# Optimization experiments

Measured on AMD Instinct MI355X. Metric: run time of the kernel, lower is better.

The kernel has to match this reference:

```python
import jax, jax.numpy as jnp
import numpy as np

N_NODES = 50000
N_EDGES = 800000
IN_CH = 10
HID = 32
HEADS = 4
OUT_CH = 64
EDIM = 1
NEG_SLOPE = 0.2  # PyG GATv2Conv default
LN_EPS = 1e-5


def _glorot(key, shape):
    fan_in, fan_out = shape[0], shape[-1]
    lim = np.sqrt(6.0 / (fan_in + fan_out))
    return jax.random.uniform(key, shape, jnp.float32, -lim, lim)


def setup_inputs() -> dict:
    key = jax.random.key(0)
    ks = jax.random.split(key, 16)
    x = jax.random.normal(ks[0], (N_NODES, IN_CH), jnp.float32)
    edge_index = jax.random.randint(ks[1], (2, N_EDGES), 0, N_NODES, jnp.int64)
    edge_attr = jax.random.normal(ks[2], (N_EDGES, EDIM), jnp.float32)
    return {
        "x": x,
        "edge_attr": edge_attr,
        "W1l": _glorot(ks[3], (IN_CH, HEADS * HID)),
        "W1r": _glorot(ks[4], (IN_CH, HEADS * HID)),
        "W1e": _glorot(ks[5], (EDIM, HEADS * HID)),
        "att1": _glorot(ks[6], (HEADS, HID)),
        "b1": jnp.zeros((HEADS * HID,), jnp.float32),
        "ln1_g": jnp.ones((HEADS * HID,), jnp.float32),
        "ln1_b": jnp.zeros((HEADS * HID,), jnp.float32),
        "W2l": _glorot(ks[7], (HEADS * HID, OUT_CH)),
        "W2r": _glorot(ks[8], (HEADS * HID, OUT_CH)),
        "W2e": _glorot(ks[9], (EDIM, OUT_CH)),
        "att2": _glorot(ks[10], (1, OUT_CH)),
        "b2": jnp.zeros((OUT_CH,), jnp.float32),
        "ln2_g": jnp.ones((OUT_CH,), jnp.float32),
        "ln2_b": jnp.zeros((OUT_CH,), jnp.float32),
        "edge_index": edge_index,
    }


def gatv2_layer(x, src, dst, edge_attr, Wl, Wr, We, att, bias, heads, ch, concat):
    # GATv2: e_ij = att . leaky_relu(Wl x_i + Wr x_j + We e_ij), softmax over j->i
    n = x.shape[0]
    xl = (x @ Wl).reshape(n, heads, ch)          # target projection [N,H,C]
    xr = (x @ Wr).reshape(n, heads, ch)          # source projection [N,H,C]
    ee = (edge_attr @ We).reshape(-1, heads, ch)  # [E,H,C]
    e = jax.nn.leaky_relu(xl[dst] + xr[src] + ee, NEG_SLOPE)  # [E,H,C]
    logit = jnp.einsum('ehc,hc->eh', e, att)     # [E,H]
    m = jax.ops.segment_max(logit, dst, num_segments=n)       # [N,H]
    expv = jnp.exp(logit - m[dst])
    denom = jax.ops.segment_sum(expv, dst, num_segments=n)    # [N,H]
    alpha = expv / denom[dst]                                  # [E,H]
    out = jax.ops.segment_sum(alpha[:, :, None] * xr[src], dst, num_segments=n)  # [N,H,C]
    out = out.reshape(n, heads * ch) if concat else out.mean(axis=1)
    return out + bias


def layer_norm(h, g, b):
    mu = h.mean(axis=-1, keepdims=True)
    var = ((h - mu) ** 2).mean(axis=-1, keepdims=True)
    return (h - mu) * jax.lax.rsqrt(var + LN_EPS) * g + b


def reference(x, edge_attr, W1l, W1r, W1e, att1, b1, ln1_g, ln1_b,
              W2l, W2r, W2e, att2, b2, ln2_g, ln2_b, edge_index):
    src, dst = edge_index[0], edge_index[1]
    h = gatv2_layer(x, src, dst, edge_attr, W1l, W1r, W1e, att1, b1, HEADS, HID, True)
    h = jax.nn.elu(layer_norm(h, ln1_g, ln1_b))
    # dropout is identity in eval mode
    h = gatv2_layer(h, src, dst, edge_attr, W2l, W2r, W2e, att2, b2, 1, OUT_CH, False)
    h = jax.nn.elu(layer_norm(h, ln2_g, ln2_b))
    return h
```

## Files before the change

kernel.cpp:

```cpp
#include <hip/hip_runtime.h>
#include <math.h>

#define NN 50000
#define NE 800000
#define IN_CH 10
#define NEGS 0.2f
#define LNEPS 1e-5f
#define LOG2E 1.4426950408889634f
#define P1_BLOCKS 12500
#define CH_BLOCKS 782
#define NBUK 196

typedef float f2 __attribute__((ext_vector_type(2)));

__device__ __forceinline__ f2 pkfma(f2 a, f2 b, f2 c) {
    return __builtin_elementwise_fma(a, b, c);
}
__device__ __forceinline__ float dppadd1(float v) {
    int r = __builtin_amdgcn_update_dpp(0, __float_as_int(v), 0xB1, 0xF, 0xF, true);
    return v + __int_as_float(r);
}
__device__ __forceinline__ float dppadd2(float v) {
    int r = __builtin_amdgcn_update_dpp(0, __float_as_int(v), 0x4E, 0xF, 0xF, true);
    return v + __int_as_float(r);
}
__device__ __forceinline__ float swzadd4(float v) {
    return v + __int_as_float(__builtin_amdgcn_ds_swizzle(__float_as_int(v), 0x101F));
}
__device__ __forceinline__ float swzadd8(float v) {
    return v + __int_as_float(__builtin_amdgcn_ds_swizzle(__float_as_int(v), 0x201F));
}
__device__ __forceinline__ float red16g(float v) {
    v = dppadd1(v); v = dppadd2(v); v = swzadd4(v); v = swzadd8(v);
    return v;
}
__device__ __forceinline__ float red32g(float v) {
    v = red16g(v);
    v += __int_as_float(__builtin_amdgcn_ds_swizzle(__float_as_int(v), 0x401F));
    return v;
}

__device__ __forceinline__ unsigned pack_bf16(float a, float b) {
    unsigned ua = __float_as_uint(a);
    unsigned ub = __float_as_uint(b);
    ua = (ua + 0x7FFFu + ((ua >> 16) & 1u)) >> 16;
    ub = (ub + 0x7FFFu + ((ub >> 16) & 1u)) & 0xFFFF0000u;
    return ua | ub;
}
__device__ __forceinline__ float bf_lo(unsigned d) { return __uint_as_float(d << 16); }
__device__ __forceinline__ float bf_hi(unsigned d) { return __uint_as_float(d & 0xFFFF0000u); }

__global__ __launch_bounds__(256) void k_proj1_hist(
    const float* __restrict__ x, const float* __restrict__ Wl,
    const float* __restrict__ Wr, float* __restrict__ xl, unsigned* __restrict__ xrb,
    const int* __restrict__ ei, int* __restrict__ bh) {
    __shared__ int h[256];
    int bI = blockIdx.x;
    if (bI < P1_BLOCKS) {
        int lane = threadIdx.x & 63;
        int n = bI * 4 + (threadIdx.x >> 6);
        int c0 = lane * 2;
        float al0 = 0.f, al1 = 0.f, ar0 = 0.f, ar1 = 0.f;
#pragma unroll
        for (int k = 0; k < IN_CH; ++k) {
            float xv = x[n * IN_CH + k];
            al0 = fmaf(xv, Wl[k * 128 + c0], al0);
            al1 = fmaf(xv, Wl[k * 128 + c0 + 1], al1);
            ar0 = fmaf(xv, Wr[k * 128 + c0], ar0);
            ar1 = fmaf(xv, Wr[k * 128 + c0 + 1], ar1);
        }
        *(float2*)&xl[(size_t)n * 128 + c0] = make_float2(al0, al1);
        xrb[(size_t)n * 64 + lane] = pack_bf16(ar0, ar1);
    } else {
        int t = threadIdx.x, b = bI - P1_BLOCKS;
        h[t] = 0;
        __syncthreads();
        int e0 = b * 1024 + t * 4;
        if (e0 < NE) {
            int4 d4 = *(const int4*)(ei + NE + e0);
            atomicAdd(&h[d4.x >> 8], 1);
            atomicAdd(&h[d4.y >> 8], 1);
            atomicAdd(&h[d4.z >> 8], 1);
            atomicAdd(&h[d4.w >> 8], 1);
        }
        __syncthreads();
        bh[b * 256 + t] = h[t];
    }
}

__global__ __launch_bounds__(256) void k_colscan(
    int* __restrict__ bh, int* __restrict__ coltotal) {
    __shared__ int sh[256];
    int t = threadIdx.x, j = blockIdx.x;
    int v[4];
    int mysum = 0;
#pragma unroll
    for (int i = 0; i < 4; ++i) {
        int r = t * 4 + i;
        v[i] = (r < CH_BLOCKS) ? bh[r * 256 + j] : 0;
        mysum += v[i];
    }
    sh[t] = mysum;
    __syncthreads();
    for (int off = 1; off < 256; off <<= 1) {
        int u = (t >= off) ? sh[t - off] : 0;
        __syncthreads();
        sh[t] += u;
        __syncthreads();
    }
    int ex = sh[t] - mysum;
#pragma unroll
    for (int i = 0; i < 4; ++i) {
        int r = t * 4 + i;
        if (r < CH_BLOCKS) { bh[r * 256 + j] = ex; ex += v[i]; }
    }
    if (t == 255) coltotal[j] = sh[255];
}

__global__ __launch_bounds__(256) void k_coarse(
    const int* __restrict__ ei, const float* __restrict__ ea,
    const int* __restrict__ bh, const int* __restrict__ coltotal,
    int2* __restrict__ coarse) {
    __shared__ int h[256];
    __shared__ int lbase[256];
    __shared__ int sh[256];
    int t = threadIdx.x, b = blockIdx.x;
    int ct = coltotal[t];
    sh[t] = ct;
    __syncthreads();
    for (int off = 1; off < 256; off <<= 1) {
        int u = (t >= off) ? sh[t - off] : 0;
        __syncthreads();
        sh[t] += u;
        __syncthreads();
    }
    h[t] = 0;
    lbase[t] = (sh[t] - ct) + bh[b * 256 + t];
    __syncthreads();
    int e0 = b * 1024 + t * 4;
    if (e0 >= NE) return;
    int4 d4 = *(const int4*)(ei + NE + e0);
    int4 s4 = *(const int4*)(ei + e0);
    float4 a4 = *(const float4*)(ea + e0);
    {
        int bk = d4.x >> 8; int r = atomicAdd(&h[bk], 1);
        coarse[lbase[bk] + r] = make_int2(s4.x | ((d4.x & 255) << 16), __float_as_int(a4.x));
    }
    {
        int bk = d4.y >> 8; int r = atomicAdd(&h[bk], 1);
        coarse[lbase[bk] + r] = make_int2(s4.y | ((d4.y & 255) << 16), __float_as_int(a4.y));
    }
    {
        int bk = d4.z >> 8; int r = atomicAdd(&h[bk], 1);
        coarse[lbase[bk] + r] = make_int2(s4.z | ((d4.z & 255) << 16), __float_as_int(a4.z));
    }
    {
        int bk = d4.w >> 8; int r = atomicAdd(&h[bk], 1);
        coarse[lbase[bk] + r] = make_int2(s4.w | ((d4.w & 255) << 16), __float_as_int(a4.w));
    }
}

__global__ __launch_bounds__(256) void k_fine(
    const int2* __restrict__ coarse, const int* __restrict__ coltotal,
    int* __restrict__ rowstart, int2* __restrict__ cpack) {
    __shared__ int cnt[256];
    __shared__ int pfx[256];
    __shared__ int sh[256];
    __shared__ int bbx[257];
    int t = threadIdx.x, b = blockIdx.x;
    int ct = coltotal[t];
    sh[t] = ct;
    __syncthreads();
    for (int off = 1; off < 256; off <<= 1) {
        int u = (t >= off) ? sh[t - off] : 0;
        __syncthreads();
        sh[t] += u;
        __syncthreads();
    }
    bbx[t] = sh[t] - ct;
    if (t == 255) bbx[256] = sh[255];
    cnt[t] = 0;
    __syncthreads();
    int lo = bbx[b], hi = bbx[b + 1];
    int ecnt = hi - lo;
    for (int i = t; i < ecnt; i += 256) {
        int dl = (coarse[lo + i].x >> 16) & 255;
        atomicAdd(&cnt[dl], 1);
    }
    __syncthreads();
    int v = cnt[t];
    sh[t] = v;
    __syncthreads();
    for (int off = 1; off < 256; off <<= 1) {
        int u = (t >= off) ? sh[t - off] : 0;
        __syncthreads();
        sh[t] += u;
        __syncthreads();
    }
    pfx[t] = sh[t] - v;
    int n0 = b * 256;
    if (n0 + t < NN) rowstart[n0 + t] = lo + (sh[t] - v);
    if (b == 0 && t == 0) rowstart[NN] = NE;
    cnt[t] = 0;
    __syncthreads();
    for (int i = t; i < ecnt; i += 256) {
        int2 c = coarse[lo + i];
        int dl = (c.x >> 16) & 255;
        int r = atomicAdd(&cnt[dl], 1);
        cpack[lo + pfx[dl] + r] = make_int2(c.x & 0xFFFF, c.y);
    }
}

__global__ __launch_bounds__(256) void k_proj2(
    const float* __restrict__ h1, const float* __restrict__ Wl,
    const float* __restrict__ Wr, float* __restrict__ xl2, unsigned* __restrict__ xr2b) {
    __shared__ float sh_h[64][36];
    __shared__ float sh_w[32][128];
    int t = threadIdx.x;
    int cg = t & 15, ng = t >> 4;
    int c0 = cg * 8;
    int nb = blockIdx.x * 64;
    float acc[4][8];
#pragma unroll
    for (int j = 0; j < 4; ++j)
#pragma unroll
        for (int i = 0; i < 8; ++i) acc[j][i] = 0.f;

    for (int kc = 0; kc < 128; kc += 32) {
#pragma unroll
        for (int i = 0; i < 2; ++i) {
            int fi = t + i * 256;
            int nl = fi >> 3, kq = fi & 7;
            int n = nb + nl;
            float4 v = make_float4(0.f, 0.f, 0.f, 0.f);
            if (n < NN) v = *(const float4*)&h1[(size_t)n * 128 + kc + kq * 4];
            *(float4*)&sh_h[nl][kq * 4] = v;
        }
#pragma unroll
        for (int i = 0; i < 4; ++i) {
            int fi = t + i * 256;
            int kl = fi >> 5, col = (fi & 31) * 4;
            const float* src = (col < 64) ? &Wl[(size_t)(kc + kl) * 64 + col]
                                          : &Wr[(size_t)(kc + kl) * 64 + col - 64];
            *(float4*)&sh_w[kl][col] = *(const float4*)src;
        }
        __syncthreads();
#pragma unroll
        for (int kl = 0; kl < 32; kl += 4) {
            float4 hv[4];
#pragma unroll
            for (int j = 0; j < 4; ++j) hv[j] = *(const float4*)&sh_h[ng + j * 16][kl];
#pragma unroll
            for (int kk = 0; kk < 4; ++kk) {
                float4 wa = *(const float4*)&sh_w[kl + kk][c0];
                float4 wb = *(const float4*)&sh_w[kl + kk][c0 + 4];
#pragma unroll
                for (int j = 0; j < 4; ++j) {
                    float hs = kk == 0 ? hv[j].x : kk == 1 ? hv[j].y : kk == 2 ? hv[j].z : hv[j].w;
                    acc[j][0] = fmaf(hs, wa.x, acc[j][0]);
                    acc[j][1] = fmaf(hs, wa.y, acc[j][1]);
                    acc[j][2] = fmaf(hs, wa.z, acc[j][2]);
                    acc[j][3] = fmaf(hs, wa.w, acc[j][3]);
                    acc[j][4] = fmaf(hs, wb.x, acc[j][4]);
                    acc[j][5] = fmaf(hs, wb.y, acc[j][5]);
                    acc[j][6] = fmaf(hs, wb.z, acc[j][6]);
                    acc[j][7] = fmaf(hs, wb.w, acc[j][7]);
                }
            }
        }
        __syncthreads();
    }
    if (cg < 8) {
#pragma unroll
        for (int j = 0; j < 4; ++j) {
            int n = nb + ng + j * 16;
            if (n < NN) {
                *(float4*)&xl2[(size_t)n * 64 + c0] =
                    make_float4(acc[j][0], acc[j][1], acc[j][2], acc[j][3]);
                *(float4*)&xl2[(size_t)n * 64 + c0 + 4] =
                    make_float4(acc[j][4], acc[j][5], acc[j][6], acc[j][7]);
            }
        }
    } else {
        int cc = c0 - 64;
#pragma unroll
        for (int j = 0; j < 4; ++j) {
            int n = nb + ng + j * 16;
            if (n < NN) {
                uint4 pk;
                pk.x = pack_bf16(acc[j][0], acc[j][1]);
                pk.y = pack_bf16(acc[j][2], acc[j][3]);
                pk.z = pack_bf16(acc[j][4], acc[j][5]);
                pk.w = pack_bf16(acc[j][6], acc[j][7]);
                *(uint4*)&xr2b[(size_t)n * 32 + (cc >> 1)] = pk;
            }
        }
    }
}


__global__ __launch_bounds__(256) void k_fused1(
    const int* __restrict__ rs, const int2* __restrict__ cpack,
    const float* __restrict__ xl, const unsigned char* __restrict__ xrb,
    const float* __restrict__ We, const float* __restrict__ att,
    const float* __restrict__ bias, const float* __restrict__ g,
    const float* __restrict__ b, float* __restrict__ h1) {
    int lane = threadIdx.x & 63;
    int n = blockIdx.x * 4 + (threadIdx.x >> 6);
    if (n >= NN) return;
    int half = lane >> 5;
    int l = lane & 31;
    int c0 = l * 4;
    unsigned loff = (unsigned)(l * 8);
    float4 xldf = *(const float4*)&xl[(size_t)n * 128 + c0];
    float4 Wef = *(const float4*)&We[c0];
    float4 atv = *(const float4*)&att[c0];
    f2 xl01 = {xldf.x, xldf.y}, xl23 = {xldf.z, xldf.w};
    f2 We01 = {Wef.x, Wef.y}, We23 = {Wef.z, Wef.w};
    f2 at6a = {atv.x * (0.6f * LOG2E), atv.y * (0.6f * LOG2E)};
    f2 at6b = {atv.z * (0.6f * LOG2E), atv.w * (0.6f * LOG2E)};
    f2 at4a = {atv.x * (0.4f * LOG2E), atv.y * (0.4f * LOG2E)};
    f2 at4b = {atv.z * (0.4f * LOG2E), atv.w * (0.4f * LOG2E)};
    int beg = rs[n], end = rs[n + 1];
    f2 a01[2] = {{0.f, 0.f}, {0.f, 0.f}};
    f2 a23[2] = {{0.f, 0.f}, {0.f, 0.f}};
    float den[2] = {0.f, 0.f};
    for (int p0 = beg; p0 < end; p0 += 8) {
        int2 pk[4];
        bool vv[4];
#pragma unroll
        for (int s = 0; s < 4; ++s) {
            int p = p0 + s * 2 + half;
            vv[s] = p < end;
            pk[s] = cpack[vv[s] ? p : end - 1];
        }
        uint2 dw[4];
#pragma unroll
        for (int s = 0; s < 4; ++s)
            dw[s] = *(const uint2*)(xrb + (unsigned)pk[s].x * 256u + loff);
#pragma unroll
        for (int s = 0; s < 4; ++s) {
            float eav = __int_as_float(pk[s].y);
            f2 x01, x23;
            x01.x = bf_lo(dw[s].x); x01.y = bf_hi(dw[s].x);
            x23.x = bf_lo(dw[s].y); x23.y = bf_hi(dw[s].y);
            f2 ev = {eav, eav};
            f2 u01 = pkfma(ev, We01, xl01) + x01;
            f2 u23 = pkfma(ev, We23, xl23) + x23;
            float dot = fmaf(at6a.x, u01.x, at4a.x * fabsf(u01.x));
            dot = fmaf(at6a.y, u01.y, fmaf(at4a.y, fabsf(u01.y), dot));
            dot = fmaf(at6b.x, u23.x, fmaf(at4b.x, fabsf(u23.x), dot));
            dot = fmaf(at6b.y, u23.y, fmaf(at4b.y, fabsf(u23.y), dot));
            dot = dppadd1(dot);
            dot = dppadd2(dot);
            dot = swzadd4(dot);
            float el = vv[s] ? exp2f(dot) : 0.f;
            int w = s & 1;
            den[w] += el;
            f2 el2 = {el, el};
            a01[w] = pkfma(el2, x01, a01[w]);
            a23[w] = pkfma(el2, x23, a23[w]);
        }
    }
    f2 s01 = a01[0] + a01[1];
    f2 s23 = a23[0] + a23[1];
    float den0 = den[0] + den[1];
    s01.x += __shfl_xor(s01.x, 32);
    s01.y += __shfl_xor(s01.y, 32);
    s23.x += __shfl_xor(s23.x, 32);
    s23.y += __shfl_xor(s23.y, 32);
    den0 += __shfl_xor(den0, 32);
    float inv = den0 > 0.f ? 1.f / den0 : 0.f;
    float4 bv = *(const float4*)&bias[c0];
    float a0 = s01.x * inv + bv.x;
    float a1 = s01.y * inv + bv.y;
    float a2 = s23.x * inv + bv.z;
    float a3 = s23.y * inv + bv.w;
    float mu = red32g(a0 + a1 + a2 + a3) * (1.f / 128.f);
    float d0 = a0 - mu, d1 = a1 - mu, d2 = a2 - mu, d3 = a3 - mu;
    float var = red32g(d0 * d0 + d1 * d1 + d2 * d2 + d3 * d3) * (1.f / 128.f);
    float rsq = rsqrtf(var + LNEPS);
    float4 gv = *(const float4*)&g[c0];
    float4 bb = *(const float4*)&b[c0];
    float o0 = d0 * rsq * gv.x + bb.x;
    float o1 = d1 * rsq * gv.y + bb.y;
    float o2 = d2 * rsq * gv.z + bb.z;
    float o3 = d3 * rsq * gv.w + bb.w;
    o0 = o0 > 0.f ? o0 : __expf(o0) - 1.f;
    o1 = o1 > 0.f ? o1 : __expf(o1) - 1.f;
    o2 = o2 > 0.f ? o2 : __expf(o2) - 1.f;
    o3 = o3 > 0.f ? o3 : __expf(o3) - 1.f;
    if (half == 0)
        *(float4*)&h1[(size_t)n * 128 + c0] = make_float4(o0, o1, o2, o3);
}

__global__ __launch_bounds__(256) void k_fused2(
    const int* __restrict__ rs, const int2* __restrict__ cpack,
    const float* __restrict__ xl2, const unsigned char* __restrict__ xr2b,
    const float* __restrict__ We, const float* __restrict__ att,
    const float* __restrict__ bias, const float* __restrict__ g,
    const float* __restrict__ b, float* __restrict__ out) {
    int lane = threadIdx.x & 63;
    int n = blockIdx.x * 4 + (threadIdx.x >> 6);
    if (n >= NN) return;
    int grp = lane >> 4;
    int l = lane & 15;
    int c0 = l * 4;
    unsigned loff = (unsigned)(l * 8);
    float4 xldf = *(const float4*)&xl2[(size_t)n * 64 + c0];
    float4 Wef = *(const float4*)&We[c0];
    float4 atv = *(const float4*)&att[c0];
    f2 xl01 = {xldf.x, xldf.y}, xl23 = {xldf.z, xldf.w};
    f2 We01 = {Wef.x, Wef.y}, We23 = {Wef.z, Wef.w};
    f2 at6a = {atv.x * (0.6f * LOG2E), atv.y * (0.6f * LOG2E)};
    f2 at6b = {atv.z * (0.6f * LOG2E), atv.w * (0.6f * LOG2E)};
    f2 at4a = {atv.x * (0.4f * LOG2E), atv.y * (0.4f * LOG2E)};
    f2 at4b = {atv.z * (0.4f * LOG2E), atv.w * (0.4f * LOG2E)};
    int beg = rs[n], end = rs[n + 1];
    f2 a01[2] = {{0.f, 0.f}, {0.f, 0.f}};
    f2 a23[2] = {{0.f, 0.f}, {0.f, 0.f}};
    float den[2] = {0.f, 0.f};
    for (int p0 = beg; p0 < end; p0 += 16) {
        int2 pk[4];
        bool vv[4];
#pragma unroll
        for (int s = 0; s < 4; ++s) {
            int p = p0 + s * 4 + grp;
            vv[s] = p < end;
            pk[s] = cpack[vv[s] ? p : end - 1];
        }
        uint2 dw[4];
#pragma unroll
        for (int s = 0; s < 4; ++s)
            dw[s] = *(const uint2*)(xr2b + (unsigned)pk[s].x * 128u + loff);
#pragma unroll
        for (int s = 0; s < 4; ++s) {
            float eav = __int_as_float(pk[s].y);
            f2 x01, x23;
            x01.x = bf_lo(dw[s].x); x01.y = bf_hi(dw[s].x);
            x23.x = bf_lo(dw[s].y); x23.y = bf_hi(dw[s].y);
            f2 ev = {eav, eav};
            f2 u01 = pkfma(ev, We01, xl01) + x01;
            f2 u23 = pkfma(ev, We23, xl23) + x23;
            float dot = fmaf(at6a.x, u01.x, at4a.x * fabsf(u01.x));
            dot = fmaf(at6a.y, u01.y, fmaf(at4a.y, fabsf(u01.y), dot));
            dot = fmaf(at6b.x, u23.x, fmaf(at4b.x, fabsf(u23.x), dot));
            dot = fmaf(at6b.y, u23.y, fmaf(at4b.y, fabsf(u23.y), dot));
            dot = dppadd1(dot);
            dot = dppadd2(dot);
            dot = swzadd4(dot);
            dot = swzadd8(dot);
            float el = vv[s] ? exp2f(dot) : 0.f;
            int w = s & 1;
            den[w] += el;
            f2 el2 = {el, el};
            a01[w] = pkfma(el2, x01, a01[w]);
            a23[w] = pkfma(el2, x23, a23[w]);
        }
    }
    f2 s01 = a01[0] + a01[1];
    f2 s23 = a23[0] + a23[1];
    float den0 = den[0] + den[1];
    s01.x += __shfl_xor(s01.x, 16); s01.x += __shfl_xor(s01.x, 32);
    s01.y += __shfl_xor(s01.y, 16); s01.y += __shfl_xor(s01.y, 32);
    s23.x += __shfl_xor(s23.x, 16); s23.x += __shfl_xor(s23.x, 32);
    s23.y += __shfl_xor(s23.y, 16); s23.y += __shfl_xor(s23.y, 32);
    den0 += __shfl_xor(den0, 16); den0 += __shfl_xor(den0, 32);
    float inv = den0 > 0.f ? 1.f / den0 : 0.f;
    float4 bv = *(const float4*)&bias[c0];
    float a0 = s01.x * inv + bv.x;
    float a1 = s01.y * inv + bv.y;
    float a2 = s23.x * inv + bv.z;
    float a3 = s23.y * inv + bv.w;
    float mu = red16g(a0 + a1 + a2 + a3) * (1.f / 64.f);
    float d0 = a0 - mu, d1 = a1 - mu, d2 = a2 - mu, d3 = a3 - mu;
    float var = red16g(d0 * d0 + d1 * d1 + d2 * d2 + d3 * d3) * (1.f / 64.f);
    float rsq = rsqrtf(var + LNEPS);
    float4 gv = *(const float4*)&g[c0];
    float4 bb = *(const float4*)&b[c0];
    float o0 = d0 * rsq * gv.x + bb.x;
    float o1 = d1 * rsq * gv.y + bb.y;
    float o2 = d2 * rsq * gv.z + bb.z;
    float o3 = d3 * rsq * gv.w + bb.w;
    o0 = o0 > 0.f ? o0 : __expf(o0) - 1.f;
    o1 = o1 > 0.f ? o1 : __expf(o1) - 1.f;
    o2 = o2 > 0.f ? o2 : __expf(o2) - 1.f;
    o3 = o3 > 0.f ? o3 : __expf(o3) - 1.f;
    if (grp == 0)
        *(float4*)&out[(size_t)n * 64 + c0] = make_float4(o0, o1, o2, o3);
}

extern "C" void kernel_launch(void* const* d_in, const int* in_sizes, int n_in,
                              void* d_out, int out_size, void* d_ws, size_t ws_size,
                              hipStream_t stream) {
    const float* x    = (const float*)d_in[0];
    const float* ea   = (const float*)d_in[1];
    const float* W1l  = (const float*)d_in[2];
    const float* W1r  = (const float*)d_in[3];
    const float* W1e  = (const float*)d_in[4];
    const float* att1 = (const float*)d_in[5];
    const float* b1   = (const float*)d_in[6];
    const float* ln1g = (const float*)d_in[7];
    const float* ln1b = (const float*)d_in[8];
    const float* W2l  = (const float*)d_in[9];
    const float* W2r  = (const float*)d_in[10];
    const float* W2e  = (const float*)d_in[11];
    const float* att2 = (const float*)d_in[12];
    const float* b2   = (const float*)d_in[13];
    const float* ln2g = (const float*)d_in[14];
    const float* ln2b = (const float*)d_in[15];
    const int*   ei   = (const int*)d_in[16];
    float* out = (float*)d_out;
    float* ws  = (float*)d_ws;

    const size_t A = (size_t)NN * 128;
    float* xl1 = ws;
    float* h1  = ws + A;
    float* xl2 = ws + 2 * A;
    unsigned* xr1b = (unsigned*)(ws + 2 * A + (size_t)NN * 64);
    unsigned* xr2b = xr1b + (size_t)NN * 64;
    int2* cpack  = (int2*)(xr2b + (size_t)NN * 32);
    int2* coarse = cpack + (size_t)NE;
    int* bh      = (int*)(coarse + (size_t)NE);
    int* coltotal= bh + (size_t)CH_BLOCKS * 256;
    int* rowstart= coltotal + 256;

    k_proj1_hist<<<P1_BLOCKS + CH_BLOCKS, 256, 0, stream>>>(x, W1l, W1r, xl1, xr1b,
                                                            ei, bh);
    k_colscan<<<256, 256, 0, stream>>>(bh, coltotal);
    k_coarse<<<CH_BLOCKS, 256, 0, stream>>>(ei, ea, bh, coltotal, coarse);
    k_fine<<<NBUK, 256, 0, stream>>>(coarse, coltotal, rowstart, cpack);

    k_fused1<<<(NN + 3) / 4, 256, 0, stream>>>(rowstart, cpack, xl1,
                                               (const unsigned char*)xr1b, W1e, att1, b1,
                                               ln1g, ln1b, h1);
    k_proj2<<<(NN + 63) / 64, 256, 0, stream>>>(h1, W2l, W2r, xl2, xr2b);
    k_fused2<<<(NN + 3) / 4, 256, 0, stream>>>(rowstart, cpack, xl2,
                                               (const unsigned char*)xr2b, W2e, att2, b2,
                                               ln2g, ln2b, out);
}
```

Measured before the change: 267.5 us.

## Hoist bucket-base scan into its own kernel, widen fine sort, use shfl reductions

Moves the 256-entry prefix scan of bucket totals, which every k_coarse and k_fine block recomputed, into a single one-block kernel that writes bucket bases. k_fine now runs 1024 threads per bucket so each block walks its edges with more parallelism. The DPP and ds_swizzle lane reductions in the attention kernels are replaced with __shfl_xor, which may compile to slower LDS-permute instructions. The change also adds one extra kernel launch to the preprocessing chain.

```diff
diff --git a/kernel.cpp b/kernel.cpp
--- a/kernel.cpp
+++ b/kernel.cpp
@@ -16,27 +16,13 @@
 __device__ __forceinline__ f2 pkfma(f2 a, f2 b, f2 c) {
     return __builtin_elementwise_fma(a, b, c);
 }
-__device__ __forceinline__ float dppadd1(float v) {
-    int r = __builtin_amdgcn_update_dpp(0, __float_as_int(v), 0xB1, 0xF, 0xF, true);
-    return v + __int_as_float(r);
-}
-__device__ __forceinline__ float dppadd2(float v) {
-    int r = __builtin_amdgcn_update_dpp(0, __float_as_int(v), 0x4E, 0xF, 0xF, true);
-    return v + __int_as_float(r);
-}
-__device__ __forceinline__ float swzadd4(float v) {
-    return v + __int_as_float(__builtin_amdgcn_ds_swizzle(__float_as_int(v), 0x101F));
-}
-__device__ __forceinline__ float swzadd8(float v) {
-    return v + __int_as_float(__builtin_amdgcn_ds_swizzle(__float_as_int(v), 0x201F));
-}
 __device__ __forceinline__ float red16g(float v) {
-    v = dppadd1(v); v = dppadd2(v); v = swzadd4(v); v = swzadd8(v);
+    v += __shfl_xor(v, 1);  v += __shfl_xor(v, 2);
+    v += __shfl_xor(v, 4);  v += __shfl_xor(v, 8);
     return v;
 }
 __device__ __forceinline__ float red32g(float v) {
-    v = red16g(v);
-    v += __int_as_float(__builtin_amdgcn_ds_swizzle(__float_as_int(v), 0x401F));
+    v = red16g(v); v += __shfl_xor(v, 16);
     return v;
 }
 
@@ -117,25 +103,32 @@
     if (t == 255) coltotal[j] = sh[255];
 }
 
+__global__ __launch_bounds__(256) void k_bb(
+    const int* __restrict__ coltotal, int* __restrict__ bb) {
+    __shared__ int sh[256];
+    int t = threadIdx.x;
+    int v = coltotal[t];
+    sh[t] = v;
+    __syncthreads();
+    for (int off = 1; off < 256; off <<= 1) {
+        int u = (t >= off) ? sh[t - off] : 0;
+        __syncthreads();
+        sh[t] += u;
+        __syncthreads();
+    }
+    bb[t] = sh[t] - v;
+    if (t == 255) bb[256] = sh[255];
+}
+
 __global__ __launch_bounds__(256) void k_coarse(
     const int* __restrict__ ei, const float* __restrict__ ea,
-    const int* __restrict__ bh, const int* __restrict__ coltotal,
+    const int* __restrict__ bh, const int* __restrict__ bb,
     int2* __restrict__ coarse) {
     __shared__ int h[256];
     __shared__ int lbase[256];
-    __shared__ int sh[256];
     int t = threadIdx.x, b = blockIdx.x;
-    int ct = coltotal[t];
-    sh[t] = ct;
-    __syncthreads();
-    for (int off = 1; off < 256; off <<= 1) {
-        int u = (t >= off) ? sh[t - off] : 0;
-        __syncthreads();
-        sh[t] += u;
-        __syncthreads();
-    }
     h[t] = 0;
-    lbase[t] = (sh[t] - ct) + bh[b * 256 + t];
+    lbase[t] = bb[t] + bh[b * 256 + t];
     __syncthreads();
     int e0 = b * 1024 + t * 4;
     if (e0 >= NE) return;
@@ -160,50 +153,40 @@
     }
 }
 
-__global__ __launch_bounds__(256) void k_fine(
-    const int2* __restrict__ coarse, const int* __restrict__ coltotal,
+__global__ __launch_bounds__(1024) void k_fine(
+    const int2* __restrict__ coarse, const int* __restrict__ bb,
     int* __restrict__ rowstart, int2* __restrict__ cpack) {
     __shared__ int cnt[256];
     __shared__ int pfx[256];
     __shared__ int sh[256];
-    __shared__ int bbx[257];
     int t = threadIdx.x, b = blockIdx.x;
-    int ct = coltotal[t];
-    sh[t] = ct;
-    __syncthreads();
-    for (int off = 1; off < 256; off <<= 1) {
-        int u = (t >= off) ? sh[t - off] : 0;
-        __syncthreads();
-        sh[t] += u;
-        __syncthreads();
-    }
-    bbx[t] = sh[t] - ct;
-    if (t == 255) bbx[256] = sh[255];
-    cnt[t] = 0;
-    __syncthreads();
-    int lo = bbx[b], hi = bbx[b + 1];
+    if (t < 256) cnt[t] = 0;
+    __syncthreads();
+    int lo = bb[b], hi = bb[b + 1];
     int ecnt = hi - lo;
-    for (int i = t; i < ecnt; i += 256) {
+    for (int i = t; i < ecnt; i += 1024) {
         int dl = (coarse[lo + i].x >> 16) & 255;
         atomicAdd(&cnt[dl], 1);
     }
     __syncthreads();
-    int v = cnt[t];
-    sh[t] = v;
+    int v = 0;
+    if (t < 256) { v = cnt[t]; sh[t] = v; }
     __syncthreads();
     for (int off = 1; off < 256; off <<= 1) {
-        int u = (t >= off) ? sh[t - off] : 0;
-        __syncthreads();
-        sh[t] += u;
-        __syncthreads();
-    }
-    pfx[t] = sh[t] - v;
-    int n0 = b * 256;
-    if (n0 + t < NN) rowstart[n0 + t] = lo + (sh[t] - v);
+        int u = (t < 256 && t >= off) ? sh[t - off] : 0;
+        __syncthreads();
+        if (t < 256) sh[t] += u;
+        __syncthreads();
+    }
+    if (t < 256) {
+        pfx[t] = sh[t] - v;
+        int n0 = b * 256;
+        if (n0 + t < NN) rowstart[n0 + t] = lo + (sh[t] - v);
+        cnt[t] = 0;
+    }
     if (b == 0 && t == 0) rowstart[NN] = NE;
-    cnt[t] = 0;
-    __syncthreads();
-    for (int i = t; i < ecnt; i += 256) {
+    __syncthreads();
+    for (int i = t; i < ecnt; i += 1024) {
         int2 c = coarse[lo + i];
         int dl = (c.x >> 16) & 255;
         int r = atomicAdd(&cnt[dl], 1);
@@ -351,9 +334,9 @@
             dot = fmaf(at6a.y, u01.y, fmaf(at4a.y, fabsf(u01.y), dot));
             dot = fmaf(at6b.x, u23.x, fmaf(at4b.x, fabsf(u23.x), dot));
             dot = fmaf(at6b.y, u23.y, fmaf(at4b.y, fabsf(u23.y), dot));
-            dot = dppadd1(dot);
-            dot = dppadd2(dot);
-            dot = swzadd4(dot);
+            dot += __shfl_xor(dot, 1);
+            dot += __shfl_xor(dot, 2);
+            dot += __shfl_xor(dot, 4);
             float el = vv[s] ? exp2f(dot) : 0.f;
             int w = s & 1;
             den[w] += el;
@@ -446,10 +429,10 @@
             dot = fmaf(at6a.y, u01.y, fmaf(at4a.y, fabsf(u01.y), dot));
             dot = fmaf(at6b.x, u23.x, fmaf(at4b.x, fabsf(u23.x), dot));
             dot = fmaf(at6b.y, u23.y, fmaf(at4b.y, fabsf(u23.y), dot));
-            dot = dppadd1(dot);
-            dot = dppadd2(dot);
-            dot = swzadd4(dot);
-            dot = swzadd8(dot);
+            dot += __shfl_xor(dot, 1);
+            dot += __shfl_xor(dot, 2);
+            dot += __shfl_xor(dot, 4);
+            dot += __shfl_xor(dot, 8);
             float el = vv[s] ? exp2f(dot) : 0.f;
             int w = s & 1;
             den[w] += el;
@@ -523,13 +506,15 @@
     int2* coarse = cpack + (size_t)NE;
     int* bh      = (int*)(coarse + (size_t)NE);
     int* coltotal= bh + (size_t)CH_BLOCKS * 256;
-    int* rowstart= coltotal + 256;
+    int* bb      = coltotal + 256;
+    int* rowstart= bb + 258;
 
     k_proj1_hist<<<P1_BLOCKS + CH_BLOCKS, 256, 0, stream>>>(x, W1l, W1r, xl1, xr1b,
                                                             ei, bh);
     k_colscan<<<256, 256, 0, stream>>>(bh, coltotal);
-    k_coarse<<<CH_BLOCKS, 256, 0, stream>>>(ei, ea, bh, coltotal, coarse);
-    k_fine<<<NBUK, 256, 0, stream>>>(coarse, coltotal, rowstart, cpack);
+    k_bb<<<1, 256, 0, stream>>>(coltotal, bb);
+    k_coarse<<<CH_BLOCKS, 256, 0, stream>>>(ei, ea, bh, bb, coarse);
+    k_fine<<<NBUK, 1024, 0, stream>>>(coarse, bb, rowstart, cpack);
 
     k_fused1<<<(NN + 3) / 4, 256, 0, stream>>>(rowstart, cpack, xl1,
                                                (const unsigned char*)xr1b, W1e, att1, b1,
```

After: 281.9 us. 1.05x slower.
